# Kernel tuning notes

Measured on AMD Instinct MI355X. Metric: run time of the kernel, lower is better.

## Reference

```python
import jax, jax.numpy as jnp
import numpy as np

B, N, M = 8, 2048, 2048
DQ = DK = DV = H = O = 1024

def setup_inputs() -> dict:
    key = jax.random.key(0)
    ks = jax.random.split(key, 10)
    input_query = jax.random.normal(ks[0], (B, N, DQ), dtype=jnp.float32)
    input_key = jax.random.normal(ks[1], (B, M, DK), dtype=jnp.float32)
    input_value = jax.random.normal(ks[2], (B, M, DV), dtype=jnp.float32)
    seq_lens = jax.random.randint(ks[3], (B,), 1, M + 1)
    seq_lens = seq_lens.at[0].set(M)  # original asserts max(seq_lens) == M
    s = 1.0 / np.sqrt(DQ)
    Wq = jax.random.normal(ks[4], (DQ, H), dtype=jnp.float32) * s
    bq = jnp.zeros((H,), dtype=jnp.float32)
    Wk = jax.random.normal(ks[5], (DK, H), dtype=jnp.float32) * s
    bk = jnp.zeros((H,), dtype=jnp.float32)
    Wv = jax.random.normal(ks[6], (DV, O), dtype=jnp.float32) * s
    bv = jnp.zeros((O,), dtype=jnp.float32)
    return {"input_query": input_query, "input_key": input_key, "input_value": input_value,
            "seq_lens": seq_lens, "Wq": Wq, "bq": bq, "Wk": Wk, "bk": bk, "Wv": Wv, "bv": bv}


def reference(input_query, input_key, input_value, seq_lens, Wq, bq, Wk, bk, Wv, bv):
    hidden_dim = Wq.shape[1]
    lq = input_query @ Wq + bq          # (B, N, H)
    lk = input_key @ Wk + bk            # (B, M, H)
    lv = input_value @ Wv + bv          # (B, M, O)
    scores = jnp.einsum('bnh,bmh->bnm', lq, lk) / jnp.sqrt(jnp.float32(hidden_dim))
    # additive mask: 0 for valid positions, finfo.min for padded (as in original)
    valid = (jnp.arange(scores.shape[-1]) < seq_lens[:, None])[:, None, :]  # (B,1,M)
    add_mask = jnp.where(valid, 0.0, jnp.finfo(scores.dtype).min)
    scores = scores + add_mask
    probs = jax.nn.softmax(scores, axis=-1)
    out = jnp.einsum('bnm,bmo->bno', probs, lv)  # dropout is identity in eval
    return out
```

## Files before the change

### kernel.cpp

```cpp
#include <hip/hip_runtime.h>
#include <hip/hip_bf16.h>

typedef unsigned short u16;
typedef __attribute__((ext_vector_type(8))) short bfrag;
typedef __attribute__((ext_vector_type(4))) float f32x4;
typedef __attribute__((ext_vector_type(8))) unsigned short us8;
typedef __attribute__((ext_vector_type(4))) unsigned short us4;

__device__ __forceinline__ u16 f2bf(float f) {
  union { float f; unsigned int u; } x; x.f = f;
  unsigned int r = x.u + 0x7fffu + ((x.u >> 16) & 1u);
  return (u16)(r >> 16);
}
__device__ __forceinline__ float bf2f(u16 u) {
  union { unsigned int u; float f; } x; x.u = ((unsigned int)u) << 16;
  return x.f;
}

__device__ __forceinline__ void gld16(const void* g, void* l) {
  __builtin_amdgcn_global_load_lds((const __attribute__((address_space(1))) void*)g,
                                   (__attribute__((address_space(3))) void*)l, 16, 0, 0);
}

__global__ __launch_bounds__(256) void transpose_w(const float* __restrict__ W0,
                                                   const float* __restrict__ W1,
                                                   const float* __restrict__ W2,
                                                   u16* __restrict__ T0,
                                                   u16* __restrict__ T1,
                                                   u16* __restrict__ T2) {
  const float* W = (blockIdx.z == 0) ? W0 : ((blockIdx.z == 1) ? W1 : W2);
  u16* T = (blockIdx.z == 0) ? T0 : ((blockIdx.z == 1) ? T1 : T2);
  __shared__ u16 tile[64][72];
  const int t = threadIdx.x;
  const int rr = t >> 4;
  const int cc = (t & 15) * 4;
  const int kbase = blockIdx.y * 64, nbase = blockIdx.x * 64;
#pragma unroll
  for (int j = 0; j < 4; ++j) {
    int kl = rr + j * 16;
    float4 v = *(const float4*)(W + (size_t)(kbase + kl) * 1024 + nbase + cc);
    tile[kl][cc + 0] = f2bf(v.x);
    tile[kl][cc + 1] = f2bf(v.y);
    tile[kl][cc + 2] = f2bf(v.z);
    tile[kl][cc + 3] = f2bf(v.w);
  }
  __syncthreads();
#pragma unroll
  for (int j = 0; j < 4; ++j) {
    int nl = rr + j * 16;
    us4 o;
    o[0] = tile[cc + 0][nl];
    o[1] = tile[cc + 1][nl];
    o[2] = tile[cc + 2][nl];
    o[3] = tile[cc + 3][nl];
    *(us4*)(T + (size_t)(nbase + nl) * 1024 + kbase + cc) = o;
  }
}

__global__ __launch_bounds__(256) void cvt_bf16(const float* __restrict__ src,
                                                u16* __restrict__ dst, int n8) {
  int i = blockIdx.x * blockDim.x + threadIdx.x;
  const int stride = gridDim.x * blockDim.x;
  for (; i < n8; i += stride) {
    const float4* p = (const float4*)(src + (size_t)i * 8);
    float4 v0 = p[0], v1 = p[1];
    us8 o;
    o[0] = f2bf(v0.x); o[1] = f2bf(v0.y); o[2] = f2bf(v0.z); o[3] = f2bf(v0.w);
    o[4] = f2bf(v1.x); o[5] = f2bf(v1.y); o[6] = f2bf(v1.z); o[7] = f2bf(v1.w);
    *(us8*)(dst + (size_t)i * 8) = o;
  }
}

template <int OUT>
__global__ __launch_bounds__(512, 2) void gemm256(const u16* __restrict__ gA,
                                                  const u16* __restrict__ gB,
                                                  const float* __restrict__ bias,
                                                  void* __restrict__ outp,
                                                  int K, int ldc,
                                                  size_t aStride, size_t bStride,
                                                  size_t cStride) {
  __shared__ u16 lds[65536];
  const int tid = threadIdx.x;

  const int gx = gridDim.x, gy = gridDim.y;
  const int nwg = gx * gy * gridDim.z;
  int orig = blockIdx.x + gx * (blockIdx.y + gy * blockIdx.z);
  {
    const int qq = nwg >> 3, rr2 = nwg & 7;
    const int xcd = orig & 7, idx = orig >> 3;
    orig = (xcd < rr2 ? xcd * (qq + 1) : rr2 * (qq + 1) + (xcd - rr2) * qq) + idx;
  }
  const int bx = orig % gx;
  const int tmp_ = orig / gx;
  const int by = tmp_ % gy, bz = tmp_ / gy;

  const u16* A = gA + (size_t)bz * aStride;
  const u16* B = gB + (size_t)bz * bStride;
  const int brow = by * 256, bcol = bx * 256;

  const int wv = tid >> 6, l = tid & 63;
  const int wm = wv >> 2, wn = wv & 3;
  const int fr = l & 15, fq = l >> 4;
  const int g0 = (fq ^ (fr & 7)) * 8;
  const int g1 = ((4 + fq) ^ (fr & 7)) * 8;

  const int srow = tid >> 3;
  const int sg = (tid & 7) ^ (srow & 7);
  const u16* aS = A + (size_t)(brow + srow) * K + sg * 8;
  const u16* bS = B + (size_t)(bcol + srow) * K + sg * 8;
  u16* const dA = lds + wv * 512;
  u16* const dB = lds + 32768 + wv * 512;

  f32x4 acc[8][4] = {};
  const int NT = K >> 6;

  auto stA = [&](int tile, int c, int buf) {
    gld16(aS + (size_t)tile * 64 + (size_t)c * 64 * K, dA + buf * 16384 + c * 4096);
  };
  auto stB = [&](int tile, int c, int buf) {
    gld16(bS + (size_t)tile * 64 + (size_t)c * 64 * K, dB + buf * 16384 + c * 4096);
  };

#pragma unroll
  for (int c = 0; c < 4; ++c) stA(0, c, 0);
#pragma unroll
  for (int c = 0; c < 4; ++c) stB(0, c, 0);
  if (NT > 1) {
    stA(1, 0, 1); stA(1, 2, 1);
    stB(1, 0, 1); stB(1, 1, 1); stB(1, 2, 1); stB(1, 3, 1);
  }

  for (int t = 0; t < NT; ++t) {
    const int cur = t & 1;
    const u16* At = lds + cur * 16384;
    const u16* Bt = lds + 32768 + cur * 16384;

    if (t + 1 < NT) asm volatile("s_waitcnt vmcnt(6)" ::: "memory");
    else            asm volatile("s_waitcnt vmcnt(0)" ::: "memory");
    __builtin_amdgcn_s_barrier();

    bfrag a[4][2], b[2][2][2];

#pragma unroll
    for (int m = 0; m < 4; ++m) {
      const u16* p = At + (wm * 128 + m * 16 + fr) * 64;
      a[m][0] = *(const bfrag*)(p + g0);
      a[m][1] = *(const bfrag*)(p + g1);
    }
#pragma unroll
    for (int n = 0; n < 2; ++n) {
      const u16* p = Bt + (wn * 64 + n * 16 + fr) * 64;
      b[0][n][0] = *(const bfrag*)(p + g0);
      b[0][n][1] = *(const bfrag*)(p + g1);
    }
    if (t + 1 < NT) { stA(t + 1, 1, cur ^ 1); stA(t + 1, 3, cur ^ 1); }
    __builtin_amdgcn_s_barrier();
    __builtin_amdgcn_s_setprio(1);
#pragma unroll
    for (int n = 0; n < 2; ++n)
#pragma unroll
      for (int m = 0; m < 4; ++m) {
        acc[m][n] = __builtin_amdgcn_mfma_f32_16x16x32_bf16(a[m][0], b[0][n][0], acc[m][n], 0, 0, 0);
        acc[m][n] = __builtin_amdgcn_mfma_f32_16x16x32_bf16(a[m][1], b[0][n][1], acc[m][n], 0, 0, 0);
      }
    __builtin_amdgcn_s_setprio(0);
    __builtin_amdgcn_s_barrier();

#pragma unroll
    for (int n = 0; n < 2; ++n) {
      const u16* p = Bt + (wn * 64 + 32 + n * 16 + fr) * 64;
      b[1][n][0] = *(const bfrag*)(p + g0);
      b[1][n][1] = *(const bfrag*)(p + g1);
    }
    if (t + 2 < NT) { stA(t + 2, 0, cur); stA(t + 2, 2, cur); }
    __builtin_amdgcn_s_barrier();
    __builtin_amdgcn_s_setprio(1);
#pragma unroll
    for (int n = 0; n < 2; ++n)
#pragma unroll
      for (int m = 0; m < 4; ++m) {
        acc[m][2 + n] = __builtin_amdgcn_mfma_f32_16x16x32_bf16(a[m][0], b[1][n][0], acc[m][2 + n], 0, 0, 0);
        acc[m][2 + n] = __builtin_amdgcn_mfma_f32_16x16x32_bf16(a[m][1], b[1][n][1], acc[m][2 + n], 0, 0, 0);
      }
    __builtin_amdgcn_s_setprio(0);
    __builtin_amdgcn_s_barrier();

#pragma unroll
    for (int m = 0; m < 4; ++m) {
      const u16* p = At + (wm * 128 + 64 + m * 16 + fr) * 64;
      a[m][0] = *(const bfrag*)(p + g0);
      a[m][1] = *(const bfrag*)(p + g1);
    }
    if (t + 2 < NT) { stB(t + 2, 0, cur); stB(t + 2, 1, cur); }
    __builtin_amdgcn_s_barrier();
    __builtin_amdgcn_s_setprio(1);
#pragma unroll
    for (int n = 0; n < 2; ++n)
#pragma unroll
      for (int m = 0; m < 4; ++m) {
        acc[4 + m][n] = __builtin_amdgcn_mfma_f32_16x16x32_bf16(a[m][0], b[0][n][0], acc[4 + m][n], 0, 0, 0);
        acc[4 + m][n] = __builtin_amdgcn_mfma_f32_16x16x32_bf16(a[m][1], b[0][n][1], acc[4 + m][n], 0, 0, 0);
      }
    __builtin_amdgcn_s_setprio(0);
    __builtin_amdgcn_s_barrier();

    if (t + 2 < NT) { stB(t + 2, 2, cur); stB(t + 2, 3, cur); }
    __builtin_amdgcn_s_setprio(1);
#pragma unroll
    for (int n = 0; n < 2; ++n)
#pragma unroll
      for (int m = 0; m < 4; ++m) {
        acc[4 + m][2 + n] = __builtin_amdgcn_mfma_f32_16x16x32_bf16(a[m][0], b[1][n][0], acc[4 + m][2 + n], 0, 0, 0);
        acc[4 + m][2 + n] = __builtin_amdgcn_mfma_f32_16x16x32_bf16(a[m][1], b[1][n][1], acc[4 + m][2 + n], 0, 0, 0);
      }
    __builtin_amdgcn_s_setprio(0);
    __builtin_amdgcn_s_barrier();
  }

#pragma unroll
  for (int mg = 0; mg < 8; ++mg) {
    const int r0 = brow + wm * 128 + mg * 16 + fq * 4;
#pragma unroll
    for (int n = 0; n < 4; ++n) {
      const int c = bcol + wn * 64 + n * 16 + fr;
      f32x4 vv = acc[mg][n];
      if constexpr (OUT == 0) {
        float bb = bias[c];
        u16* C = (u16*)outp;
#pragma unroll
        for (int j = 0; j < 4; ++j) C[(size_t)(r0 + j) * ldc + c] = f2bf(vv[j] + bb);
      } else if constexpr (OUT == 1) {
        u16* C = (u16*)outp + (size_t)bz * cStride;
#pragma unroll
        for (int j = 0; j < 4; ++j) C[(size_t)(r0 + j) * ldc + c] = f2bf(vv[j] * 0.03125f);
      } else if constexpr (OUT == 2) {
        float bb = bias[c];
        const int bz2 = r0 >> 11, mm = r0 & 2047;
        us4 o;
#pragma unroll
        for (int j = 0; j < 4; ++j) o[j] = f2bf(vv[j] + bb);
        *(us4*)((u16*)outp + ((size_t)bz2 * 1024 + c) * 2048 + mm) = o;
      } else {
        float* C = (float*)outp + (size_t)bz * cStride;
#pragma unroll
        for (int j = 0; j < 4; ++j) C[(size_t)(r0 + j) * ldc + c] = vv[j];
      }
    }
  }
}

__global__ __launch_bounds__(256) void softmax_mask(u16* __restrict__ probs,
                                                    const int* __restrict__ seq) {
  const int bid = blockIdx.x;
  const int b = bid >> 11, n = bid & 2047;
  const int len = seq[b];
  u16* row = probs + ((size_t)b * 2048 + n) * 2048;
  const int t = threadIdx.x;
  const int w = t >> 6, l = t & 63;

  us8 sv = *(const us8*)(row + t * 8);
  float vals[8];
  float vmax = -1e30f;
#pragma unroll
  for (int e = 0; e < 8; ++e) {
    int m = t * 8 + e;
    float x = bf2f(sv[e]);
    vals[e] = (m < len) ? x : -1e30f;
    vmax = fmaxf(vmax, vals[e]);
  }
#pragma unroll
  for (int o = 32; o > 0; o >>= 1) vmax = fmaxf(vmax, __shfl_xor(vmax, o, 64));
  __shared__ float sm[4], ss[4];
  if (l == 0) sm[w] = vmax;
  __syncthreads();
  vmax = fmaxf(fmaxf(sm[0], sm[1]), fmaxf(sm[2], sm[3]));

  float ev[8];
  float sum = 0.f;
#pragma unroll
  for (int e = 0; e < 8; ++e) {
    int m = t * 8 + e;
    float p = (m < len) ? __expf(vals[e] - vmax) : 0.f;
    ev[e] = p;
    sum += p;
  }
#pragma unroll
  for (int o = 32; o > 0; o >>= 1) sum += __shfl_xor(sum, o, 64);
  if (l == 0) ss[w] = sum;
  __syncthreads();
  sum = ss[0] + ss[1] + ss[2] + ss[3];
  float inv = 1.f / sum;
  us8 ov;
#pragma unroll
  for (int e = 0; e < 8; ++e) ov[e] = f2bf(ev[e] * inv);
  *(us8*)(row + t * 8) = ov;
}

extern "C" void kernel_launch(void* const* d_in, const int* in_sizes, int n_in,
                              void* d_out, int out_size, void* d_ws, size_t ws_size,
                              hipStream_t stream) {
  const float* q   = (const float*)d_in[0];
  const float* k   = (const float*)d_in[1];
  const float* v   = (const float*)d_in[2];
  const int*   seq = (const int*)d_in[3];
  const float* Wq  = (const float*)d_in[4];
  const float* bq  = (const float*)d_in[5];
  const float* Wk  = (const float*)d_in[6];
  const float* bk  = (const float*)d_in[7];
  const float* Wv  = (const float*)d_in[8];
  const float* bv  = (const float*)d_in[9];
  float* out = (float*)d_out;

  u16* ws = (u16*)d_ws;
  u16* wtq = ws;
  u16* wtk = wtq + (size_t)1024 * 1024;
  u16* wtv = wtk + (size_t)1024 * 1024;
  u16* lq  = wtv + (size_t)1024 * 1024;
  u16* lk  = lq + (size_t)16384 * 1024;
  u16* lvt = lk + (size_t)16384 * 1024;
  u16* probs = lvt + (size_t)16384 * 1024;
  u16* cbuf = probs;

  const size_t S21 = (size_t)2048 * 1024;
  const size_t S22 = (size_t)2048 * 2048;

  transpose_w<<<dim3(16, 16, 3), 256, 0, stream>>>(Wq, Wk, Wv, wtq, wtk, wtv);

  cvt_bf16<<<dim3(2048), 256, 0, stream>>>(q, cbuf, 2097152);
  gemm256<0><<<dim3(4, 64, 1), 512, 0, stream>>>(cbuf, wtq, bq, lq, 1024, 1024, 0, 0, 0);
  cvt_bf16<<<dim3(2048), 256, 0, stream>>>(k, cbuf, 2097152);
  gemm256<0><<<dim3(4, 64, 1), 512, 0, stream>>>(cbuf, wtk, bk, lk, 1024, 1024, 0, 0, 0);
  cvt_bf16<<<dim3(2048), 256, 0, stream>>>(v, cbuf, 2097152);
  gemm256<2><<<dim3(4, 64, 1), 512, 0, stream>>>(cbuf, wtv, bv, lvt, 1024, 1024, 0, 0, 0);

  gemm256<1><<<dim3(8, 8, 8), 512, 0, stream>>>(lq, lk, nullptr, probs, 1024, 2048, S21, S21, S22);
  softmax_mask<<<dim3(16384), 256, 0, stream>>>(probs, seq);
  gemm256<3><<<dim3(4, 8, 8), 512, 0, stream>>>(probs, lvt, nullptr, out, 2048, 1024, S22, S21, S21);
}
```

Measured before the change: 335.1 us.

## Skip masked key tiles in score, softmax and PV GEMMs using seq_lens

The QK^T GEMM now exits early for 256-column tiles lying entirely beyond the batch's sequence length. The PV GEMM truncates its K loop to the 64-aligned valid length. Softmax skips loading masked columns and writes only up to the 64-aligned length, which keeps the truncated PV reads consistent. The GEMM main loop also gains explicit lgkmcnt waits plus sched barriers after the LDS fragment loads, and drops the trailing barrier. Dropping that barrier could risk a race on the double buffer.

```diff
diff --git a/kernel.cpp b/kernel.cpp
--- a/kernel.cpp
+++ b/kernel.cpp
@@ -78,7 +78,8 @@
                                                   void* __restrict__ outp,
                                                   int K, int ldc,
                                                   size_t aStride, size_t bStride,
-                                                  size_t cStride) {
+                                                  size_t cStride,
+                                                  const int* __restrict__ seq) {
   __shared__ u16 lds[65536];
   const int tid = threadIdx.x;
 
@@ -98,6 +99,17 @@
   const u16* B = gB + (size_t)bz * bStride;
   const int brow = by * 256, bcol = bx * 256;
 
+  const int NT = K >> 6;
+  int NTe = NT;
+  if constexpr (OUT == 1) {
+    if (bcol >= seq[bz]) return;
+  }
+  if constexpr (OUT == 3) {
+    const int len = seq[bz];
+    const int nt2 = (len + 63) >> 6;
+    NTe = nt2 < NT ? nt2 : NT;
+  }
+
   const int wv = tid >> 6, l = tid & 63;
   const int wm = wv >> 2, wn = wv & 3;
   const int fr = l & 15, fq = l >> 4;
@@ -112,7 +124,6 @@
   u16* const dB = lds + 32768 + wv * 512;
 
   f32x4 acc[8][4] = {};
-  const int NT = K >> 6;
 
   auto stA = [&](int tile, int c, int buf) {
     gld16(aS + (size_t)tile * 64 + (size_t)c * 64 * K, dA + buf * 16384 + c * 4096);
@@ -125,18 +136,18 @@
   for (int c = 0; c < 4; ++c) stA(0, c, 0);
 #pragma unroll
   for (int c = 0; c < 4; ++c) stB(0, c, 0);
-  if (NT > 1) {
+  if (NTe > 1) {
     stA(1, 0, 1); stA(1, 2, 1);
     stB(1, 0, 1); stB(1, 1, 1); stB(1, 2, 1); stB(1, 3, 1);
   }
 
-  for (int t = 0; t < NT; ++t) {
+  for (int t = 0; t < NTe; ++t) {
     const int cur = t & 1;
     const u16* At = lds + cur * 16384;
     const u16* Bt = lds + 32768 + cur * 16384;
 
-    if (t + 1 < NT) asm volatile("s_waitcnt vmcnt(6)" ::: "memory");
-    else            asm volatile("s_waitcnt vmcnt(0)" ::: "memory");
+    if (t + 1 < NTe) asm volatile("s_waitcnt vmcnt(6)" ::: "memory");
+    else             asm volatile("s_waitcnt vmcnt(0)" ::: "memory");
     __builtin_amdgcn_s_barrier();
 
     bfrag a[4][2], b[2][2][2];
@@ -153,8 +164,10 @@
       b[0][n][0] = *(const bfrag*)(p + g0);
       b[0][n][1] = *(const bfrag*)(p + g1);
     }
-    if (t + 1 < NT) { stA(t + 1, 1, cur ^ 1); stA(t + 1, 3, cur ^ 1); }
-    __builtin_amdgcn_s_barrier();
+    if (t + 1 < NTe) { stA(t + 1, 1, cur ^ 1); stA(t + 1, 3, cur ^ 1); }
+    __builtin_amdgcn_s_barrier();
+    asm volatile("s_waitcnt lgkmcnt(0)" ::: "memory");
+    __builtin_amdgcn_sched_barrier(0);
     __builtin_amdgcn_s_setprio(1);
 #pragma unroll
     for (int n = 0; n < 2; ++n)
@@ -172,8 +185,10 @@
       b[1][n][0] = *(const bfrag*)(p + g0);
       b[1][n][1] = *(const bfrag*)(p + g1);
     }
-    if (t + 2 < NT) { stA(t + 2, 0, cur); stA(t + 2, 2, cur); }
-    __builtin_amdgcn_s_barrier();
+    if (t + 2 < NTe) { stA(t + 2, 0, cur); stA(t + 2, 2, cur); }
+    __builtin_amdgcn_s_barrier();
+    asm volatile("s_waitcnt lgkmcnt(0)" ::: "memory");
+    __builtin_amdgcn_sched_barrier(0);
     __builtin_amdgcn_s_setprio(1);
 #pragma unroll
     for (int n = 0; n < 2; ++n)
@@ -191,8 +206,10 @@
       a[m][0] = *(const bfrag*)(p + g0);
       a[m][1] = *(const bfrag*)(p + g1);
     }
-    if (t + 2 < NT) { stB(t + 2, 0, cur); stB(t + 2, 1, cur); }
-    __builtin_amdgcn_s_barrier();
+    if (t + 2 < NTe) { stB(t + 2, 0, cur); stB(t + 2, 1, cur); }
+    __builtin_amdgcn_s_barrier();
+    asm volatile("s_waitcnt lgkmcnt(0)" ::: "memory");
+    __builtin_amdgcn_sched_barrier(0);
     __builtin_amdgcn_s_setprio(1);
 #pragma unroll
     for (int n = 0; n < 2; ++n)
@@ -204,7 +221,7 @@
     __builtin_amdgcn_s_setprio(0);
     __builtin_amdgcn_s_barrier();
 
-    if (t + 2 < NT) { stB(t + 2, 2, cur); stB(t + 2, 3, cur); }
+    if (t + 2 < NTe) { stB(t + 2, 2, cur); stB(t + 2, 3, cur); }
     __builtin_amdgcn_s_setprio(1);
 #pragma unroll
     for (int n = 0; n < 2; ++n)
@@ -214,7 +231,6 @@
         acc[4 + m][2 + n] = __builtin_amdgcn_mfma_f32_16x16x32_bf16(a[m][1], b[1][n][1], acc[4 + m][2 + n], 0, 0, 0);
       }
     __builtin_amdgcn_s_setprio(0);
-    __builtin_amdgcn_s_barrier();
   }
 
 #pragma unroll
@@ -254,11 +270,13 @@
   const int bid = blockIdx.x;
   const int b = bid >> 11, n = bid & 2047;
   const int len = seq[b];
+  const int len64 = (len + 63) & ~63;
   u16* row = probs + ((size_t)b * 2048 + n) * 2048;
   const int t = threadIdx.x;
   const int w = t >> 6, l = t & 63;
 
-  us8 sv = *(const us8*)(row + t * 8);
+  us8 sv = {};
+  if (t * 8 < len) sv = *(const us8*)(row + t * 8);
   float vals[8];
   float vmax = -1e30f;
 #pragma unroll
@@ -290,10 +308,12 @@
   __syncthreads();
   sum = ss[0] + ss[1] + ss[2] + ss[3];
   float inv = 1.f / sum;
-  us8 ov;
-#pragma unroll
-  for (int e = 0; e < 8; ++e) ov[e] = f2bf(ev[e] * inv);
-  *(us8*)(row + t * 8) = ov;
+  if (t * 8 < len64) {
+    us8 ov;
+#pragma unroll
+    for (int e = 0; e < 8; ++e) ov[e] = f2bf(ev[e] * inv);
+    *(us8*)(row + t * 8) = ov;
+  }
 }
 
 extern "C" void kernel_launch(void* const* d_in, const int* in_sizes, int n_in,
@@ -327,13 +347,13 @@
   transpose_w<<<dim3(16, 16, 3), 256, 0, stream>>>(Wq, Wk, Wv, wtq, wtk, wtv);
 
   cvt_bf16<<<dim3(2048), 256, 0, stream>>>(q, cbuf, 2097152);
-  gemm256<0><<<dim3(4, 64, 1), 512, 0, stream>>>(cbuf, wtq, bq, lq, 1024, 1024, 0, 0, 0);
+  gemm256<0><<<dim3(4, 64, 1), 512, 0, stream>>>(cbuf, wtq, bq, lq, 1024, 1024, 0, 0, 0, nullptr);
   cvt_bf16<<<dim3(2048), 256, 0, stream>>>(k, cbuf, 2097152);
-  gemm256<0><<<dim3(4, 64, 1), 512, 0, stream>>>(cbuf, wtk, bk, lk, 1024, 1024, 0, 0, 0);
+  gemm256<0><<<dim3(4, 64, 1), 512, 0, stream>>>(cbuf, wtk, bk, lk, 1024, 1024, 0, 0, 0, nullptr);
   cvt_bf16<<<dim3(2048), 256, 0, stream>>>(v, cbuf, 2097152);
-  gemm256<2><<<dim3(4, 64, 1), 512, 0, stream>>>(cbuf, wtv, bv, lvt, 1024, 1024, 0, 0, 0);
-
-  gemm256<1><<<dim3(8, 8, 8), 512, 0, stream>>>(lq, lk, nullptr, probs, 1024, 2048, S21, S21, S22);
+  gemm256<2><<<dim3(4, 64, 1), 512, 0, stream>>>(cbuf, wtv, bv, lvt, 1024, 1024, 0, 0, 0, nullptr);
+
+  gemm256<1><<<dim3(8, 8, 8), 512, 0, stream>>>(lq, lk, nullptr, probs, 1024, 2048, S21, S21, S22, seq);
   softmax_mask<<<dim3(16384), 256, 0, stream>>>(probs, seq);
-  gemm256<3><<<dim3(4, 8, 8), 512, 0, stream>>>(probs, lvt, nullptr, out, 2048, 1024, S22, S21, S21);
-}
+  gemm256<3><<<dim3(4, 8, 8), 512, 0, stream>>>(probs, lvt, nullptr, out, 2048, 1024, S22, S21, S21, seq);
+}
```

Result: faster. 325.9 us (-2.7%).
